# Optimization experiments

Measured on AMD Instinct MI355X. Metric: run time of the kernel, lower is better.

## Reference

```python
import jax, jax.numpy as jnp
import numpy as np

HIDDEN = 256
HEADS = 8
HEAD_DIM = HIDDEN // HEADS
RBF_DIM = 50
EPS = 1e-5


def setup_inputs() -> dict:
    key = jax.random.key(0)
    ks = jax.random.split(key, 16)
    L, P = 1024, 2048
    s = 0.02
    inp = {
        "lig_h": jax.random.normal(ks[0], (L, HIDDEN), jnp.float32),
        "prot_h": jax.random.normal(ks[1], (P, HIDDEN), jnp.float32),
        "rbf": jax.random.uniform(ks[2], (L, P, RBF_DIM), jnp.float32),
        "L": L,
        "P": P,
        "Wq": jax.random.normal(ks[3], (HIDDEN, HIDDEN), jnp.float32) * s,
        "bq": jnp.zeros((HIDDEN,), jnp.float32),
        "Wk": jax.random.normal(ks[4], (HIDDEN, HIDDEN), jnp.float32) * s,
        "bk": jnp.zeros((HIDDEN,), jnp.float32),
        "Wv": jax.random.normal(ks[5], (HIDDEN, HIDDEN), jnp.float32) * s,
        "bv": jnp.zeros((HIDDEN,), jnp.float32),
        "Wrbf": jax.random.normal(ks[6], (RBF_DIM, HEADS), jnp.float32) * s,
        "brbf": jnp.zeros((HEADS,), jnp.float32),
        "Wo": jax.random.normal(ks[7], (HIDDEN, HIDDEN), jnp.float32) * s,
        "bo": jnp.zeros((HIDDEN,), jnp.float32),
        "gamma": jnp.ones((HIDDEN,), jnp.float32),
        "beta": jnp.zeros((HIDDEN,), jnp.float32),
    }
    return inp


def reference(lig_h, prot_h, rbf, L, P, Wq, bq, Wk, bk, Wv, bv, Wrbf, brbf, Wo, bo, gamma, beta):
    scale = float(HEAD_DIM) ** 0.5
    Q = (lig_h @ Wq + bq).reshape(L, HEADS, HEAD_DIM)
    K = (prot_h @ Wk + bk).reshape(P, HEADS, HEAD_DIM)
    V = (prot_h @ Wv + bv).reshape(P, HEADS, HEAD_DIM)
    attn = jnp.einsum('lhd,phd->lph', Q, K) / scale
    dist_bias = rbf @ Wrbf + brbf          # [L, P, H]
    attn = attn + dist_bias
    attn_weights = jax.nn.softmax(attn, axis=1)  # over P (protein) axis
    attended = jnp.einsum('lph,phd->lhd', attn_weights, V).reshape(L, HIDDEN)
    y = lig_h + attended @ Wo + bo
    mu = jnp.mean(y, axis=-1, keepdims=True)
    var = jnp.var(y, axis=-1, keepdims=True)
    lig_h_out = (y - mu) * jax.lax.rsqrt(var + EPS) * gamma + beta
    return (lig_h_out, attn_weights)
```

## Files before the change

kernel.cpp:

```cpp
#include <hip/hip_runtime.h>
#include <hip/hip_bf16.h>

#define L_SZ 1024
#define P_SZ 2048
#define HID 256
#define NH 8
#define HD 32
#define NRBF 50
#define CH 32
#define NCH 64

typedef unsigned int uint32;
typedef _Float16 half2_t __attribute__((ext_vector_type(2)));
typedef __fp16 fp16x2_t __attribute__((ext_vector_type(2)));

__constant__ float kINV_SCALE = 0.17677669529663687f;

static __device__ __forceinline__ unsigned short f2h(float f) {
    union { _Float16 h; unsigned short u; } x; x.h = (_Float16)f; return x.u;
}
static __device__ __forceinline__ float h2f(unsigned short u) {
    union { unsigned short u; _Float16 h; } x; x.u = u; return (float)x.h;
}
static __device__ __forceinline__ half2_t u2h2(uint32 u) {
    union { uint32 u; half2_t h; } x; x.u = u; return x.h;
}
static __device__ __forceinline__ half2_t pk2h(float a, float b) {
    union { fp16x2_t p; half2_t h; } x; x.p = __builtin_amdgcn_cvt_pkrtz(a, b); return x.h;
}

static __device__ __forceinline__ void g2l16(const void* g, void* l) {
    __builtin_amdgcn_global_load_lds(
        (__attribute__((address_space(1))) void*)(void*)g,
        (__attribute__((address_space(3))) void*)l, 16, 0, 0);
}
static __device__ __forceinline__ void g2l4(const void* g, void* l) {
    __builtin_amdgcn_global_load_lds(
        (__attribute__((address_space(1))) void*)(void*)g,
        (__attribute__((address_space(3))) void*)l, 4, 0, 0);
}

#define WAITV0 asm volatile("s_waitcnt vmcnt(0)" ::: "memory")
#define WAITV1 asm volatile("s_waitcnt vmcnt(1)" ::: "memory")
#define CFENCE asm volatile("" ::: "memory")

__global__ __launch_bounds__(64) void k_proj(
    const float* __restrict__ lig, const float* __restrict__ prot,
    const float* __restrict__ Wq, const float* __restrict__ bq,
    const float* __restrict__ Wk, const float* __restrict__ bk,
    const float* __restrict__ Wv, const float* __restrict__ bv,
    float* __restrict__ Qf, unsigned short* __restrict__ Kb,
    unsigned short* __restrict__ Vb)
{
    __shared__ float As[8 * HID];
    const int t = threadIdx.x;
    const int r0 = blockIdx.x * 8;

    const float* src; const float* W; const float* bias; int mode; int row0;
    if (r0 < L_SZ)            { src = lig  + (size_t)r0 * HID;               W = Wq; bias = bq; mode = 0; row0 = r0; }
    else if (r0 < L_SZ + P_SZ){ src = prot + (size_t)(r0 - L_SZ) * HID;      W = Wk; bias = bk; mode = 1; row0 = r0 - L_SZ; }
    else                      { src = prot + (size_t)(r0 - L_SZ - P_SZ)*HID; W = Wv; bias = bv; mode = 2; row0 = r0 - L_SZ - P_SZ; }

    float4* A4 = (float4*)As;
    const float4* S4 = (const float4*)src;
    #pragma unroll
    for (int j = 0; j < 8; ++j) A4[t + j * 64] = S4[t + j * 64];
    __syncthreads();

    float acc[8][4];
    #pragma unroll
    for (int r = 0; r < 8; ++r)
        #pragma unroll
        for (int c = 0; c < 4; ++c) acc[r][c] = 0.f;

    for (int k4 = 0; k4 < 64; ++k4) {
        float4 av[8];
        #pragma unroll
        for (int r = 0; r < 8; ++r) av[r] = A4[r * 64 + k4];
        #pragma unroll
        for (int kk = 0; kk < 4; ++kk) {
            const float* wr = W + (size_t)(k4 * 4 + kk) * HID + t;
            #pragma unroll
            for (int c = 0; c < 4; ++c) {
                float wv = wr[c * 64];
                #pragma unroll
                for (int r = 0; r < 8; ++r)
                    acc[r][c] += ((const float*)&av[r])[kk] * wv;
            }
        }
    }

    #pragma unroll
    for (int c = 0; c < 4; ++c) {
        const int col = t + c * 64;
        const float bb = bias[col];
        #pragma unroll
        for (int r = 0; r < 8; ++r) {
            float v = acc[r][c] + bb;
            size_t idx = (size_t)(row0 + r) * HID + col;
            if (mode == 0)      Qf[idx] = v;
            else if (mode == 1) Kb[idx] = f2h(v);
            else                Vb[idx] = f2h(v);
        }
    }
}

__global__ __launch_bounds__(256, 3) void k_attn(
    const float* __restrict__ rbf, const float* __restrict__ Qf,
    const unsigned short* __restrict__ Kb, const unsigned short* __restrict__ Vb,
    const float* __restrict__ Wrbf, const float* __restrict__ brbf,
    float* __restrict__ attn_out, float* __restrict__ att_ws)
{
    __shared__ __align__(16) char sm[47680];
    char* rbfB  = sm + 32768;
    char* wbufB = sm + 45568;
    float* red  = (float*)(sm + 47616);

    const int t = threadIdx.x;
    const int lane = t & 63;
    const int wv = t >> 6;
    const int r = t & 31;
    const int h = t >> 5;
    const int l = blockIdx.x;
    char* aoB = (char*)attn_out + (size_t)l * (P_SZ * NH * 4);

    auto stageKV = [&](const unsigned short* src, int c, char* dst) {
        const char* gb = (const char*)src + (size_t)c * (CH * 512);
        #pragma unroll
        for (int k = 0; k < 4; ++k) {
            int s = wv * 4 + k;
            int row = s * 2 + (lane >> 5);
            int off = ((lane & 31) ^ (row & 31)) << 4;
            g2l16(gb + row * 512 + off, dst + s * 1024);
        }
    };
    auto stageRBF = [&](int c, char* dst) {
        const char* gb = (const char*)rbf + (size_t)l * 409600 + (size_t)c * 6400;
        g2l16(gb + wv * 1024 + (lane << 4), dst + wv * 1024);
        if (wv == 0)      g2l16(gb + 4096 + (lane << 4), dst + 4096);
        else if (wv == 1) g2l16(gb + 5120 + (lane << 4), dst + 5120);
        else if (wv == 2) g2l4 (gb + 6144 + (lane << 2), dst + 6144);
    };

    half2_t wrb[25];
    #pragma unroll
    for (int j = 0; j < 25; ++j)
        wrb[j] = pk2h(Wrbf[(2 * j) * NH + h], Wrbf[(2 * j + 1) * NH + h]);
    const float bh = brbf[h];

    half2_t qp[16];
    {
        const float* qq = Qf + (size_t)l * HID + h * HD;
        #pragma unroll
        for (int n = 0; n < 16; ++n)
            qp[n] = pk2h(qq[2 * n], qq[2 * n + 1]);
    }

    stageKV(Kb, 0, sm);
    stageRBF(0, rbfB);

    float mx = -3.0e38f, sme = 0.f;
    for (int c = 0; c < NCH; ++c) {
        if (c == 0) { WAITV0; } else { WAITV1; }
        __builtin_amdgcn_s_barrier();
        CFENCE;
        const int cb = c & 1;
        char* kb = sm + cb * 16384;
        char* rb = rbfB + cb * 6400;
        if (c + 1 < NCH) {
            stageKV(Kb, c + 1, sm + (cb ^ 1) * 16384);
            stageRBF(c + 1, rbfB + (cb ^ 1) * 6400);
        }
        float b0 = bh, b1 = 0.f;
        const char* rrow = rb + r * 200;
        #pragma unroll
        for (int j = 0; j < 12; ++j) {
            float2 v0 = *(const float2*)(rrow + (2 * j) * 8);
            float2 v1 = *(const float2*)(rrow + (2 * j + 1) * 8);
            b0 = __builtin_amdgcn_fdot2(pk2h(v0.x, v0.y), wrb[2 * j], b0, false);
            b1 = __builtin_amdgcn_fdot2(pk2h(v1.x, v1.y), wrb[2 * j + 1], b1, false);
        }
        {
            float2 v = *(const float2*)(rrow + 24 * 8);
            b0 = __builtin_amdgcn_fdot2(pk2h(v.x, v.y), wrb[24], b0, false);
        }
        float qk0 = 0.f, qk1 = 0.f;
        const char* krow = kb + r * 512;
        #pragma unroll
        for (int jw = 0; jw < 2; ++jw) {
            int offA = (h * 64 + jw * 16) ^ (r << 4);
            int offB = (h * 64 + (jw + 2) * 16) ^ (r << 4);
            uint4 ka = *(const uint4*)(krow + offA);
            uint4 kbv = *(const uint4*)(krow + offB);
            qk0 = __builtin_amdgcn_fdot2(u2h2(ka.x),  qp[jw * 4 + 0], qk0, false);
            qk1 = __builtin_amdgcn_fdot2(u2h2(kbv.x), qp[(jw + 2) * 4 + 0], qk1, false);
            qk0 = __builtin_amdgcn_fdot2(u2h2(ka.y),  qp[jw * 4 + 1], qk0, false);
            qk1 = __builtin_amdgcn_fdot2(u2h2(kbv.y), qp[(jw + 2) * 4 + 1], qk1, false);
            qk0 = __builtin_amdgcn_fdot2(u2h2(ka.z),  qp[jw * 4 + 2], qk0, false);
            qk1 = __builtin_amdgcn_fdot2(u2h2(kbv.z), qp[(jw + 2) * 4 + 2], qk1, false);
            qk0 = __builtin_amdgcn_fdot2(u2h2(ka.w),  qp[jw * 4 + 3], qk0, false);
            qk1 = __builtin_amdgcn_fdot2(u2h2(kbv.w), qp[(jw + 2) * 4 + 3], qk1, false);
        }
        float lg = (qk0 + qk1) * kINV_SCALE + (b0 + b1);
        float nm = fmaxf(mx, lg);
        sme = sme * __expf(mx - nm) + __expf(lg - nm);
        mx = nm;
        *(unsigned short*)(aoB + (c * CH + r) * 16 + h * 2) = f2h(lg);
    }

    #pragma unroll
    for (int msk = 1; msk <= 16; msk <<= 1) {
        float om = __shfl_xor(mx, msk);
        float os = __shfl_xor(sme, msk);
        float nm = fmaxf(mx, om);
        sme = sme * __expf(mx - nm) + os * __expf(om - nm);
        mx = nm;
    }
    if ((t & 31) == 0) { red[h * 2] = mx; red[h * 2 + 1] = 1.f / sme; }

    __syncthreads();

    {
        stageKV(Vb, 0, sm);
        if (wv == 0) g2l16(aoB + (lane << 4), wbufB);

        const int h3 = t >> 5;
        const int dq = (t >> 3) & 3;
        const int ps = t & 7;
        const int vinner = h3 * 64 + dq * 16;
        const float mh = red[h3 * 2];
        const float ih = red[h3 * 2 + 1];
        float acc[8] = {0.f, 0.f, 0.f, 0.f, 0.f, 0.f, 0.f, 0.f};
        for (int c = 0; c < NCH; ++c) {
            WAITV0;
            __builtin_amdgcn_s_barrier();
            CFENCE;
            const int cb = c & 1;
            char* vb = sm + cb * 16384;
            if (c + 1 < NCH) stageKV(Vb, c + 1, sm + (cb ^ 1) * 16384);
            if (((c & 1) == 0) && (c + 2 < NCH) && wv == 0) {
                int pr = (c >> 1) + 1;
                g2l16(aoB + pr * 1024 + (lane << 4), wbufB + (pr & 1) * 1024);
            }
            const char* wp = wbufB + ((c >> 1) & 1) * 1024 + (c & 1) * 512;
            #pragma unroll
            for (int m = 0; m < 4; ++m) {
                int rr = m * 8 + ps;
                unsigned short lgr = *(const unsigned short*)(wp + rr * 16 + h3 * 2);
                float w = __expf(h2f(lgr) - mh) * ih;
                int off = vinner ^ (rr << 4);
                uint4 vvv = *(const uint4*)(vb + rr * 512 + off);
                half2_t x0 = u2h2(vvv.x), x1 = u2h2(vvv.y), x2 = u2h2(vvv.z), x3 = u2h2(vvv.w);
                acc[0] += w * (float)x0.x; acc[1] += w * (float)x0.y;
                acc[2] += w * (float)x1.x; acc[3] += w * (float)x1.y;
                acc[4] += w * (float)x2.x; acc[5] += w * (float)x2.y;
                acc[6] += w * (float)x3.x; acc[7] += w * (float)x3.y;
            }
        }
        #pragma unroll
        for (int d = 0; d < 8; ++d) {
            acc[d] += __shfl_xor(acc[d], 1);
            acc[d] += __shfl_xor(acc[d], 2);
            acc[d] += __shfl_xor(acc[d], 4);
        }
        if (ps == 0) {
            float* dst = att_ws + (size_t)l * HID + h3 * HD + dq * 8;
            *(float4*)dst       = make_float4(acc[0], acc[1], acc[2], acc[3]);
            *(float4*)(dst + 4) = make_float4(acc[4], acc[5], acc[6], acc[7]);
        }
    }
    __syncthreads();

    {
        const int hA = 2 * (t & 3);
        const float mA = red[hA * 2],     iA = red[hA * 2 + 1];
        const float mB = red[hA * 2 + 2], iB = red[hA * 2 + 3];
        for (int n = 31; n >= 0; --n) {
            int j = t + n * 256;
            uint32 a = *(const uint32*)(aoB + 4 * j);
            float w0 = __expf(h2f((unsigned short)(a & 0xffffu)) - mA) * iA;
            float w1 = __expf(h2f((unsigned short)(a >> 16))     - mB) * iB;
            __syncthreads();
            *(float2*)(aoB + 8 * (size_t)j) = make_float2(w0, w1);
        }
    }
}

__global__ __launch_bounds__(256) void k_out(
    const float* __restrict__ att, const float* __restrict__ lig,
    const float* __restrict__ Wo, const float* __restrict__ bo,
    const float* __restrict__ gamma, const float* __restrict__ beta,
    float* __restrict__ out)
{
    __shared__ float a[HID];
    __shared__ float red[8];
    const int l = blockIdx.x, t = threadIdx.x;
    if (t < 64) ((float4*)a)[t] = ((const float4*)(att + (size_t)l * HID))[t];
    __syncthreads();

    float acc = bo[t];
    for (int k4 = 0; k4 < 64; ++k4) {
        float4 av = ((float4*)a)[k4];
        const float* wr = Wo + (size_t)(k4 * 4) * HID + t;
        acc += av.x * wr[0];
        acc += av.y * wr[HID];
        acc += av.z * wr[2 * HID];
        acc += av.w * wr[3 * HID];
    }
    float y = lig[(size_t)l * HID + t] + acc;

    float s = y, sq = y * y;
    #pragma unroll
    for (int msk = 1; msk < 64; msk <<= 1) {
        s  += __shfl_xor(s, msk);
        sq += __shfl_xor(sq, msk);
    }
    const int lane = t & 63, wvi = t >> 6;
    if (lane == 0) { red[wvi * 2] = s; red[wvi * 2 + 1] = sq; }
    __syncthreads();
    float ts = red[0] + red[2] + red[4] + red[6];
    float tq = red[1] + red[3] + red[5] + red[7];
    float mu = ts * (1.0f / HID);
    float var = tq * (1.0f / HID) - mu * mu;
    out[(size_t)l * HID + t] = (y - mu) * rsqrtf(var + 1e-5f) * gamma[t] + beta[t];
}

extern "C" void kernel_launch(void* const* d_in, const int* in_sizes, int n_in,
                              void* d_out, int out_size, void* d_ws, size_t ws_size,
                              hipStream_t stream)
{
    (void)in_sizes; (void)n_in; (void)out_size; (void)ws_size;

    const float* lig   = (const float*)d_in[0];
    const float* prot  = (const float*)d_in[1];
    const float* rbf   = (const float*)d_in[2];
    const float* Wq    = (const float*)d_in[5];
    const float* bq    = (const float*)d_in[6];
    const float* Wk    = (const float*)d_in[7];
    const float* bk    = (const float*)d_in[8];
    const float* Wv    = (const float*)d_in[9];
    const float* bv    = (const float*)d_in[10];
    const float* Wrbf  = (const float*)d_in[11];
    const float* brbf  = (const float*)d_in[12];
    const float* Wo    = (const float*)d_in[13];
    const float* bo    = (const float*)d_in[14];
    const float* gamma = (const float*)d_in[15];
    const float* beta  = (const float*)d_in[16];

    float* out0 = (float*)d_out;
    float* attn = (float*)d_out + (size_t)L_SZ * HID;

    char* ws = (char*)d_ws;
    float*          Qf     = (float*)ws;
    unsigned short* Kb     = (unsigned short*)(ws + (1u << 20));
    unsigned short* Vb     = (unsigned short*)(ws + (2u << 20));
    float*          att_ws = (float*)(ws + (3u << 20));

    hipLaunchKernelGGL(k_proj, dim3((L_SZ + 2 * P_SZ) / 8), dim3(64), 0, stream,
                       lig, prot, Wq, bq, Wk, bk, Wv, bv, Qf, Kb, Vb);
    hipLaunchKernelGGL(k_attn, dim3(L_SZ), dim3(256), 0, stream,
                       rbf, Qf, Kb, Vb, Wrbf, brbf, attn, att_ws);
    hipLaunchKernelGGL(k_out, dim3(L_SZ), dim3(256), 0, stream,
                       att_ws, lig, Wo, bo, gamma, beta, out0);
}
```

Before: 335.1 us.

## Fuse PV accumulation into QK pass with lazy online-softmax rescaling

Merges the second pass over V into the first QK/bias loop. V is staged alongside K in shared memory and each thread keeps a 32-float output accumulator. Rescaling happens only when the running max grows by more than 8, and the partials are reduced across the 32 row-lanes through a transposed shared-memory buffer. This removes the separate V loop, its barriers and the re-read and re-exponentiation of logits, at the cost of more registers and LDS, so the occupancy hint drops from 3 to 2 blocks.

```diff
diff --git a/kernel.cpp b/kernel.cpp
--- a/kernel.cpp
+++ b/kernel.cpp
@@ -105,16 +105,16 @@
     }
 }
 
-__global__ __launch_bounds__(256, 3) void k_attn(
+__global__ __launch_bounds__(256, 2) void k_attn(
     const float* __restrict__ rbf, const float* __restrict__ Qf,
     const unsigned short* __restrict__ Kb, const unsigned short* __restrict__ Vb,
     const float* __restrict__ Wrbf, const float* __restrict__ brbf,
     float* __restrict__ attn_out, float* __restrict__ att_ws)
 {
-    __shared__ __align__(16) char sm[47680];
-    char* rbfB  = sm + 32768;
-    char* wbufB = sm + 45568;
-    float* red  = (float*)(sm + 47616);
+    __shared__ __align__(16) char sm[78400];
+    char* vBB  = sm + 32768;
+    char* rbfB = sm + 65536;
+    float* red = (float*)(sm + 78336);
 
     const int t = threadIdx.x;
     const int lane = t & 63;
@@ -157,18 +157,25 @@
     }
 
     stageKV(Kb, 0, sm);
+    stageKV(Vb, 0, vBB);
     stageRBF(0, rbfB);
 
     float mx = -3.0e38f, sme = 0.f;
+    float O[32];
+    #pragma unroll
+    for (int d = 0; d < 32; ++d) O[d] = 0.f;
+
     for (int c = 0; c < NCH; ++c) {
         if (c == 0) { WAITV0; } else { WAITV1; }
         __builtin_amdgcn_s_barrier();
         CFENCE;
         const int cb = c & 1;
         char* kb = sm + cb * 16384;
+        char* vb = vBB + cb * 16384;
         char* rb = rbfB + cb * 6400;
         if (c + 1 < NCH) {
             stageKV(Kb, c + 1, sm + (cb ^ 1) * 16384);
+            stageKV(Vb, c + 1, vBB + (cb ^ 1) * 16384);
             stageRBF(c + 1, rbfB + (cb ^ 1) * 6400);
         }
         float b0 = bh, b1 = 0.f;
@@ -202,74 +209,59 @@
             qk1 = __builtin_amdgcn_fdot2(u2h2(kbv.w), qp[(jw + 2) * 4 + 3], qk1, false);
         }
         float lg = (qk0 + qk1) * kINV_SCALE + (b0 + b1);
-        float nm = fmaxf(mx, lg);
-        sme = sme * __expf(mx - nm) + __expf(lg - nm);
-        mx = nm;
+
+        if (lg > mx + 8.0f) {
+            float e = __expf(mx - lg);
+            sme *= e;
+            #pragma unroll
+            for (int d = 0; d < 32; ++d) O[d] *= e;
+            mx = lg;
+        }
+        float w = __expf(lg - mx);
+        sme += w;
+
+        const char* vrow = vb + r * 512;
+        #pragma unroll
+        for (int q = 0; q < 4; ++q) {
+            int off = (h * 64 + q * 16) ^ (r << 4);
+            uint4 vvv = *(const uint4*)(vrow + off);
+            half2_t x0 = u2h2(vvv.x), x1 = u2h2(vvv.y), x2 = u2h2(vvv.z), x3 = u2h2(vvv.w);
+            O[q * 8 + 0] += w * (float)x0.x; O[q * 8 + 1] += w * (float)x0.y;
+            O[q * 8 + 2] += w * (float)x1.x; O[q * 8 + 3] += w * (float)x1.y;
+            O[q * 8 + 4] += w * (float)x2.x; O[q * 8 + 5] += w * (float)x2.y;
+            O[q * 8 + 6] += w * (float)x3.x; O[q * 8 + 7] += w * (float)x3.y;
+        }
+
         *(unsigned short*)(aoB + (c * CH + r) * 16 + h * 2) = f2h(lg);
     }
-
-    #pragma unroll
-    for (int msk = 1; msk <= 16; msk <<= 1) {
-        float om = __shfl_xor(mx, msk);
-        float os = __shfl_xor(sme, msk);
-        float nm = fmaxf(mx, om);
-        sme = sme * __expf(mx - nm) + os * __expf(om - nm);
-        mx = nm;
-    }
-    if ((t & 31) == 0) { red[h * 2] = mx; red[h * 2 + 1] = 1.f / sme; }
+    WAITV0;
+
+    float mg = mx;
+    #pragma unroll
+    for (int msk = 1; msk <= 16; msk <<= 1) mg = fmaxf(mg, __shfl_xor(mg, msk));
+    float e = __expf(mx - mg);
+    sme *= e;
+    #pragma unroll
+    for (int msk = 1; msk <= 16; msk <<= 1) sme += __shfl_xor(sme, msk);
+    float inv = 1.0f / sme;
+    if (r == 0) { red[h * 2] = mg; red[h * 2 + 1] = inv; }
+    const float scl = e * inv;
 
     __syncthreads();
 
     {
-        stageKV(Vb, 0, sm);
-        if (wv == 0) g2l16(aoB + (lane << 4), wbufB);
-
-        const int h3 = t >> 5;
-        const int dq = (t >> 3) & 3;
-        const int ps = t & 7;
-        const int vinner = h3 * 64 + dq * 16;
-        const float mh = red[h3 * 2];
-        const float ih = red[h3 * 2 + 1];
-        float acc[8] = {0.f, 0.f, 0.f, 0.f, 0.f, 0.f, 0.f, 0.f};
-        for (int c = 0; c < NCH; ++c) {
-            WAITV0;
-            __builtin_amdgcn_s_barrier();
-            CFENCE;
-            const int cb = c & 1;
-            char* vb = sm + cb * 16384;
-            if (c + 1 < NCH) stageKV(Vb, c + 1, sm + (cb ^ 1) * 16384);
-            if (((c & 1) == 0) && (c + 2 < NCH) && wv == 0) {
-                int pr = (c >> 1) + 1;
-                g2l16(aoB + pr * 1024 + (lane << 4), wbufB + (pr & 1) * 1024);
-            }
-            const char* wp = wbufB + ((c >> 1) & 1) * 1024 + (c & 1) * 512;
-            #pragma unroll
-            for (int m = 0; m < 4; ++m) {
-                int rr = m * 8 + ps;
-                unsigned short lgr = *(const unsigned short*)(wp + rr * 16 + h3 * 2);
-                float w = __expf(h2f(lgr) - mh) * ih;
-                int off = vinner ^ (rr << 4);
-                uint4 vvv = *(const uint4*)(vb + rr * 512 + off);
-                half2_t x0 = u2h2(vvv.x), x1 = u2h2(vvv.y), x2 = u2h2(vvv.z), x3 = u2h2(vvv.w);
-                acc[0] += w * (float)x0.x; acc[1] += w * (float)x0.y;
-                acc[2] += w * (float)x1.x; acc[3] += w * (float)x1.y;
-                acc[4] += w * (float)x2.x; acc[5] += w * (float)x2.y;
-                acc[6] += w * (float)x3.x; acc[7] += w * (float)x3.y;
-            }
-        }
-        #pragma unroll
-        for (int d = 0; d < 8; ++d) {
-            acc[d] += __shfl_xor(acc[d], 1);
-            acc[d] += __shfl_xor(acc[d], 2);
-            acc[d] += __shfl_xor(acc[d], 4);
-        }
-        if (ps == 0) {
-            float* dst = att_ws + (size_t)l * HID + h3 * HD + dq * 8;
-            *(float4*)dst       = make_float4(acc[0], acc[1], acc[2], acc[3]);
-            *(float4*)(dst + 4) = make_float4(acc[4], acc[5], acc[6], acc[7]);
-        }
-    }
-    __syncthreads();
+        float* otr = (float*)sm;
+        #pragma unroll
+        for (int d = 0; d < 32; ++d)
+            otr[h * 1024 + r * 32 + ((d + r) & 31)] = O[d] * scl;
+        __syncthreads();
+        const int hh = t >> 5, dd = t & 31;
+        float a = 0.f;
+        #pragma unroll
+        for (int rr = 0; rr < 32; ++rr)
+            a += otr[hh * 1024 + rr * 32 + ((dd + rr) & 31)];
+        att_ws[(size_t)l * HID + hh * HD + dd] = a;
+    }
 
     {
         const int hA = 2 * (t & 3);
```

Measured after the change: 273.8 us. 1.22x faster.
